# Performance work log

Hardware: AMD Instinct MI355X
Metric: run time of the kernel (lower is better)

## Reference

```python
import jax, jax.numpy as jnp
import numpy as np

INPUT_DIM = 64
LATENT_DIM = 128
B, N = 16, 8192
SQRT3 = float(np.sqrt(3.0))
SQRT5 = float(np.sqrt(5.0))
PATH_COEFF = float(1.0 / np.sqrt(INPUT_DIM))  # e3nn 'element' path norm, w3j(0,l,l)=I/sqrt(2l+1)


def _spherical_harmonics_lmax2(pos):
    """e3nn o3.spherical_harmonics(lmax=2, normalize=True, normalization='component').
    Returns (sh0 [..],  sh1 [..,3], sh2 [..,5])."""
    n = pos * jax.lax.rsqrt(jnp.sum(pos * pos, axis=-1, keepdims=True))
    x, y, z = n[..., 0], n[..., 1], n[..., 2]
    sh0 = jnp.ones_like(x)
    sh1 = SQRT3 * n  # component norm: sqrt(3) * unit vector, order (x,y,z)
    # l=2 block (component norm = sqrt(5) * norm-normalized polynomials)
    sh2 = SQRT5 * jnp.stack([
        SQRT3 * x * z,
        SQRT3 * x * y,
        y * y - 0.5 * (x * x + z * z),
        SQRT3 * y * z,
        (SQRT3 / 2.0) * (z * z - x * x),
    ], axis=-1)
    return sh0, sh1, sh2


def setup_inputs() -> dict:
    key = jax.random.key(0)
    k1, k2, k3, k4 = jax.random.split(key, 4)
    features = jax.random.normal(k1, (B, N, INPUT_DIM), dtype=jnp.float32)
    pos = jax.random.normal(k2, (B, N, 3), dtype=jnp.float32)
    # e3nn FullyConnectedTensorProduct weights ~ N(0,1); one [u,w] matrix per path
    W0 = jax.random.normal(k3, (INPUT_DIM, LATENT_DIM), dtype=jnp.float32)  # 0e x 0e -> 0e
    W1 = jax.random.normal(k4, (INPUT_DIM, LATENT_DIM), dtype=jnp.float32)  # 0e x 1o -> 1o
    return {"features": features, "pos": pos, "W0": W0, "W1": W1}


def reference(features, pos, W0, W1):
    sh0, sh1, sh2 = _spherical_harmonics_lmax2(pos)  # sh2 has no output path (dropped)
    # scalar path: out[b,n,w] = coeff * sum_u feat[b,n,u] W0[u,w] * sh0
    scalars = PATH_COEFF * jnp.einsum('bnu,uw->bnw', features, W0) * sh0[..., None]
    # vector path: out[b,n,w,k] = coeff * (feat @ W1)[b,n,w] * sh1[b,n,k]
    vec = PATH_COEFF * jnp.einsum('bnu,uw->bnw', features, W1)
    vectors = vec[..., :, None] * sh1[..., None, :]  # [B,N,LATENT,3]
    latent = jnp.concatenate(
        [scalars, vectors.reshape(*vectors.shape[:-2], LATENT_DIM * 3)], axis=-1
    )  # [B, N, LATENT + 3*LATENT]
    return jnp.mean(latent, axis=1)  # [B, 4*LATENT]
```

## Files before the change

### kernel.cpp

```cpp
#include <hip/hip_runtime.h>

#define B_ 16
#define N_ 8192
#define U_ 64
#define W_ 128
#define BLOCKS_PER_B 32
#define ROWS_PER_BLOCK (N_ / BLOCKS_PER_B)
#define NPROD (B_ * BLOCKS_PER_B)
#define NFIN  B_
#define GRID_ (NPROD + NFIN)
#define SENT 0x5AC3F00Du

typedef float f32x4 __attribute__((ext_vector_type(4)));


__global__ __launch_bounds__(256, 2) void so3_single_kernel(
    const float* __restrict__ feat,
    const float* __restrict__ pos,
    const float* __restrict__ W0,
    const float* __restrict__ W1,
    float* __restrict__ out,
    float* __restrict__ ws)
{
    const int blk = blockIdx.x;
    const int tid = threadIdx.x;
    unsigned* flags = (unsigned*)(ws + (size_t)NPROD * 256);

    if (blk < NPROD) {
        const int b     = blk / BLOCKS_PER_B;
        const int chunk = blk % BLOCKS_PER_B;
        const int row0  = chunk * ROWS_PER_BLOCK;
        const int grp   = tid & 15;
        const int rsub  = tid >> 4;

        const f32x4* fbase = (const f32x4*)(feat + (size_t)b * N_ * U_);

        f32x4 fb[16];
        #pragma unroll
        for (int it = 0; it < 16; ++it) {
            const int nl = it * 16 + rsub;
            fb[it] = __builtin_nontemporal_load(
                &fbase[(size_t)(row0 + nl) * 16 + grp]);
        }

        __shared__ f32x4 nlds[ROWS_PER_BLOCK];
        {
            const float* p = pos + ((size_t)b * N_ + row0 + tid) * 3;
            const float px = p[0], py = p[1], pz = p[2];
            const float inv = rsqrtf(px * px + py * py + pz * pz);
            f32x4 v;
            v.x = px * inv; v.y = py * inv; v.z = pz * inv; v.w = 1.0f;
            nlds[tid] = v;
        }
        __syncthreads();

        float acc[4][4] = {{0.f,0.f,0.f,0.f},{0.f,0.f,0.f,0.f},
                           {0.f,0.f,0.f,0.f},{0.f,0.f,0.f,0.f}};

        #pragma unroll
        for (int it = 0; it < 16; ++it) {
            const int nl = it * 16 + rsub;
            const f32x4 f  = fb[it];
            const f32x4 nv = nlds[nl];
            #pragma unroll
            for (int k = 0; k < 4; ++k) {
                const float nk = (k == 0) ? nv.x : (k == 1) ? nv.y
                               : (k == 2) ? nv.z : nv.w;
                acc[0][k] = fmaf(f.x, nk, acc[0][k]);
                acc[1][k] = fmaf(f.y, nk, acc[1][k]);
                acc[2][k] = fmaf(f.z, nk, acc[2][k]);
                acc[3][k] = fmaf(f.w, nk, acc[3][k]);
            }
        }

        __shared__ float lds[256][17];
        #pragma unroll
        for (int i = 0; i < 4; ++i) {
            lds[tid][i * 4 + 0] = acc[i][0];
            lds[tid][i * 4 + 1] = acc[i][1];
            lds[tid][i * 4 + 2] = acc[i][2];
            lds[tid][i * 4 + 3] = acc[i][3];
        }
        __syncthreads();

        const int u    = tid >> 2;
        const int j    = tid & 3;
        const int ug   = u >> 2;
        const int sub  = u & 3;
        const int slot = (j == 0) ? (sub * 4 + 3) : (sub * 4 + (j - 1));
        float s = 0.f;
        #pragma unroll
        for (int src = 0; src < 16; ++src) {
            const int t = (src & 3) * 64 + (src >> 2) * 16 + ug;
            s += lds[t][slot];
        }

        (void)__hip_atomic_exchange(&ws[(size_t)blk * 256 + tid], s,
                                    __ATOMIC_RELAXED, __HIP_MEMORY_SCOPE_AGENT);
        asm volatile("s_waitcnt vmcnt(0)" ::: "memory");
        __syncthreads();
        if (tid == 0)
            (void)__hip_atomic_exchange(&flags[blk], SENT,
                                        __ATOMIC_RELAXED, __HIP_MEMORY_SCOPE_AGENT);
        return;
    }

    const int b = blk - NPROD;

    if (tid < BLOCKS_PER_B) {
        while (__hip_atomic_load(&flags[b * BLOCKS_PER_B + tid],
                                 __ATOMIC_RELAXED,
                                 __HIP_MEMORY_SCOPE_AGENT) != SENT)
            __builtin_amdgcn_s_sleep(1);
    }
    __syncthreads();
    if (tid < BLOCKS_PER_B)
        (void)__hip_atomic_exchange(&flags[b * BLOCKS_PER_B + tid], 0u,
                                    __ATOMIC_RELAXED, __HIP_MEMORY_SCOPE_AGENT);

    float s = 0.f;
    {
        const float* base = ws + (size_t)b * BLOCKS_PER_B * 256;
        #pragma unroll
        for (int c = 0; c < BLOCKS_PER_B; ++c)
            s += __hip_atomic_load(&base[(size_t)c * 256 + tid],
                                   __ATOMIC_RELAXED, __HIP_MEMORY_SCOPE_AGENT);
    }
    __shared__ float sm[256];
    sm[tid] = s;
    __syncthreads();

    const float scaleS = 0.125f / (float)N_;
    const float scaleV = 0.125f * 1.7320508075688772f / (float)N_;

    #pragma unroll
    for (int half = 0; half < 2; ++half) {
        const int o = tid + half * 256;
        float acc = 0.f;
        if (o < 128) {
            #pragma unroll
            for (int u = 0; u < 64; ++u) acc += sm[u * 4 + 0] * W0[u * 128 + o];
            out[b * 512 + o] = acc * scaleS;
        } else {
            const int idx = o - 128;
            const int w = idx / 3;
            const int k = idx - 3 * w;
            #pragma unroll
            for (int u = 0; u < 64; ++u) acc += sm[u * 4 + 1 + k] * W1[u * 128 + w];
            out[b * 512 + 128 + idx] = acc * scaleV;
        }
    }
}

extern "C" void kernel_launch(void* const* d_in, const int* in_sizes, int n_in,
                              void* d_out, int out_size, void* d_ws, size_t ws_size,
                              hipStream_t stream) {
    const float* feat = (const float*)d_in[0];
    const float* pos  = (const float*)d_in[1];
    const float* W0   = (const float*)d_in[2];
    const float* W1   = (const float*)d_in[3];
    float* out = (float*)d_out;
    float* ws  = (float*)d_ws;

    so3_single_kernel<<<GRID_, 256, 0, stream>>>(feat, pos, W0, W1, out, ws);
}
```

Before: 12.60 us.

## Replace spin-waiting finalizer blocks with a last-arriving-block reduction

Drops the 16 dedicated finalizer blocks that polled flags with sleeps. After publishing its partial sums, each producer block now checks all 32 flags for its batch with one wavefront ballot. Whichever block sees every flag set does the cross-block reduction and the W0/W1 projection. This removes the polling latency and the extra resident blocks, at the cost of a flag read in every block. Under relaxed ordering, more than one block may occasionally run the (idempotent) finalization.

```diff
diff --git a/kernel.cpp b/kernel.cpp
--- a/kernel.cpp
+++ b/kernel.cpp
@@ -6,9 +6,7 @@
 #define W_ 128
 #define BLOCKS_PER_B 32
 #define ROWS_PER_BLOCK (N_ / BLOCKS_PER_B)
-#define NPROD (B_ * BLOCKS_PER_B)
-#define NFIN  B_
-#define GRID_ (NPROD + NFIN)
+#define GRID_ (B_ * BLOCKS_PER_B)
 #define SENT 0x5AC3F00Du
 
 typedef float f32x4 __attribute__((ext_vector_type(4)));
@@ -24,65 +22,65 @@
 {
     const int blk = blockIdx.x;
     const int tid = threadIdx.x;
-    unsigned* flags = (unsigned*)(ws + (size_t)NPROD * 256);
+    unsigned* flags = (unsigned*)(ws + (size_t)GRID_ * 256);
 
-    if (blk < NPROD) {
-        const int b     = blk / BLOCKS_PER_B;
-        const int chunk = blk % BLOCKS_PER_B;
-        const int row0  = chunk * ROWS_PER_BLOCK;
-        const int grp   = tid & 15;
-        const int rsub  = tid >> 4;
+    const int b     = blk / BLOCKS_PER_B;
+    const int chunk = blk % BLOCKS_PER_B;
+    const int row0  = chunk * ROWS_PER_BLOCK;
+    const int grp   = tid & 15;
+    const int rsub  = tid >> 4;
 
-        const f32x4* fbase = (const f32x4*)(feat + (size_t)b * N_ * U_);
+    const f32x4* fbase = (const f32x4*)(feat + (size_t)b * N_ * U_);
 
-        f32x4 fb[16];
+    f32x4 fb[16];
+    #pragma unroll
+    for (int it = 0; it < 16; ++it) {
+        const int nl = it * 16 + rsub;
+        fb[it] = __builtin_nontemporal_load(
+            &fbase[(size_t)(row0 + nl) * 16 + grp]);
+    }
+
+    __shared__ f32x4 nlds[ROWS_PER_BLOCK];
+    {
+        const float* p = pos + ((size_t)b * N_ + row0 + tid) * 3;
+        const float px = p[0], py = p[1], pz = p[2];
+        const float inv = rsqrtf(px * px + py * py + pz * pz);
+        f32x4 v;
+        v.x = px * inv; v.y = py * inv; v.z = pz * inv; v.w = 1.0f;
+        nlds[tid] = v;
+    }
+    __syncthreads();
+
+    float acc[4][4] = {{0.f,0.f,0.f,0.f},{0.f,0.f,0.f,0.f},
+                       {0.f,0.f,0.f,0.f},{0.f,0.f,0.f,0.f}};
+
+    #pragma unroll
+    for (int it = 0; it < 16; ++it) {
+        const int nl = it * 16 + rsub;
+        const f32x4 f  = fb[it];
+        const f32x4 nv = nlds[nl];
         #pragma unroll
-        for (int it = 0; it < 16; ++it) {
-            const int nl = it * 16 + rsub;
-            fb[it] = __builtin_nontemporal_load(
-                &fbase[(size_t)(row0 + nl) * 16 + grp]);
+        for (int k = 0; k < 4; ++k) {
+            const float nk = (k == 0) ? nv.x : (k == 1) ? nv.y
+                           : (k == 2) ? nv.z : nv.w;
+            acc[0][k] = fmaf(f.x, nk, acc[0][k]);
+            acc[1][k] = fmaf(f.y, nk, acc[1][k]);
+            acc[2][k] = fmaf(f.z, nk, acc[2][k]);
+            acc[3][k] = fmaf(f.w, nk, acc[3][k]);
         }
+    }
 
-        __shared__ f32x4 nlds[ROWS_PER_BLOCK];
-        {
-            const float* p = pos + ((size_t)b * N_ + row0 + tid) * 3;
-            const float px = p[0], py = p[1], pz = p[2];
-            const float inv = rsqrtf(px * px + py * py + pz * pz);
-            f32x4 v;
-            v.x = px * inv; v.y = py * inv; v.z = pz * inv; v.w = 1.0f;
-            nlds[tid] = v;
-        }
-        __syncthreads();
+    __shared__ float lds[256][17];
+    #pragma unroll
+    for (int i = 0; i < 4; ++i) {
+        lds[tid][i * 4 + 0] = acc[i][0];
+        lds[tid][i * 4 + 1] = acc[i][1];
+        lds[tid][i * 4 + 2] = acc[i][2];
+        lds[tid][i * 4 + 3] = acc[i][3];
+    }
+    __syncthreads();
 
-        float acc[4][4] = {{0.f,0.f,0.f,0.f},{0.f,0.f,0.f,0.f},
-                           {0.f,0.f,0.f,0.f},{0.f,0.f,0.f,0.f}};
-
-        #pragma unroll
-        for (int it = 0; it < 16; ++it) {
-            const int nl = it * 16 + rsub;
-            const f32x4 f  = fb[it];
-            const f32x4 nv = nlds[nl];
-            #pragma unroll
-            for (int k = 0; k < 4; ++k) {
-                const float nk = (k == 0) ? nv.x : (k == 1) ? nv.y
-                               : (k == 2) ? nv.z : nv.w;
-                acc[0][k] = fmaf(f.x, nk, acc[0][k]);
-                acc[1][k] = fmaf(f.y, nk, acc[1][k]);
-                acc[2][k] = fmaf(f.z, nk, acc[2][k]);
-                acc[3][k] = fmaf(f.w, nk, acc[3][k]);
-            }
-        }
-
-        __shared__ float lds[256][17];
-        #pragma unroll
-        for (int i = 0; i < 4; ++i) {
-            lds[tid][i * 4 + 0] = acc[i][0];
-            lds[tid][i * 4 + 1] = acc[i][1];
-            lds[tid][i * 4 + 2] = acc[i][2];
-            lds[tid][i * 4 + 3] = acc[i][3];
-        }
-        __syncthreads();
-
+    {
         const int u    = tid >> 2;
         const int j    = tid & 3;
         const int ug   = u >> 2;
@@ -102,32 +100,35 @@
         if (tid == 0)
             (void)__hip_atomic_exchange(&flags[blk], SENT,
                                         __ATOMIC_RELAXED, __HIP_MEMORY_SCOPE_AGENT);
-        return;
     }
 
-    const int b = blk - NPROD;
-
-    if (tid < BLOCKS_PER_B) {
-        while (__hip_atomic_load(&flags[b * BLOCKS_PER_B + tid],
-                                 __ATOMIC_RELAXED,
-                                 __HIP_MEMORY_SCOPE_AGENT) != SENT)
-            __builtin_amdgcn_s_sleep(1);
+    __shared__ unsigned s_win;
+    if (tid < 64) {
+        asm volatile("s_waitcnt vmcnt(0)" ::: "memory");
+        unsigned ok = 1u;
+        if (tid < BLOCKS_PER_B)
+            ok = (__hip_atomic_load(&flags[(b << 5) + tid], __ATOMIC_RELAXED,
+                                    __HIP_MEMORY_SCOPE_AGENT) == SENT) ? 1u : 0u;
+        const unsigned long long mask = __ballot(ok == 1u);
+        if (tid == 0) s_win = (mask == ~0ull) ? 1u : 0u;
     }
     __syncthreads();
+    if (!s_win) return;
+
     if (tid < BLOCKS_PER_B)
-        (void)__hip_atomic_exchange(&flags[b * BLOCKS_PER_B + tid], 0u,
+        (void)__hip_atomic_exchange(&flags[(b << 5) + tid], 0u,
                                     __ATOMIC_RELAXED, __HIP_MEMORY_SCOPE_AGENT);
 
-    float s = 0.f;
+    float s2 = 0.f;
     {
-        const float* base = ws + (size_t)b * BLOCKS_PER_B * 256;
+        const float* base = ws + (size_t)(b << 5) * 256;
         #pragma unroll
         for (int c = 0; c < BLOCKS_PER_B; ++c)
-            s += __hip_atomic_load(&base[(size_t)c * 256 + tid],
-                                   __ATOMIC_RELAXED, __HIP_MEMORY_SCOPE_AGENT);
+            s2 += __hip_atomic_load(&base[(size_t)c * 256 + tid],
+                                    __ATOMIC_RELAXED, __HIP_MEMORY_SCOPE_AGENT);
     }
     __shared__ float sm[256];
-    sm[tid] = s;
+    sm[tid] = s2;
     __syncthreads();
 
     const float scaleS = 0.125f / (float)N_;
@@ -136,18 +137,18 @@
     #pragma unroll
     for (int half = 0; half < 2; ++half) {
         const int o = tid + half * 256;
-        float acc = 0.f;
+        float a = 0.f;
         if (o < 128) {
             #pragma unroll
-            for (int u = 0; u < 64; ++u) acc += sm[u * 4 + 0] * W0[u * 128 + o];
-            out[b * 512 + o] = acc * scaleS;
+            for (int u = 0; u < 64; ++u) a += sm[u * 4 + 0] * W0[u * 128 + o];
+            out[b * 512 + o] = a * scaleS;
         } else {
             const int idx = o - 128;
             const int w = idx / 3;
             const int k = idx - 3 * w;
             #pragma unroll
-            for (int u = 0; u < 64; ++u) acc += sm[u * 4 + 1 + k] * W1[u * 128 + w];
-            out[b * 512 + 128 + idx] = acc * scaleV;
+            for (int u = 0; u < 64; ++u) a += sm[u * 4 + 1 + k] * W1[u * 128 + w];
+            out[b * 512 + 128 + idx] = a * scaleV;
         }
     }
 }
```

After: 14.86 us. +17.9%, slower.
